# Optimization experiments

Hardware: AMD Instinct MI355X
Metric: run time of the kernel (lower is better)

The kernel has to match this reference:

```python
import jax, jax.numpy as jnp
import numpy as np

TOP_K = 2  # num_experts_per_tok


def setup_inputs() -> dict:
    key = jax.random.key(0)
    ks = jax.random.split(key, 4)
    B, S, H, I, E = 4, 2048, 2048, 4096, 8
    std = 0.02
    hidden_states = jax.random.normal(ks[0], (B, S, H), dtype=jnp.float32)
    gate_w = jax.random.normal(ks[1], (E, H), dtype=jnp.float32) * std   # nn.Linear weight [E,H]
    wfc = jax.random.normal(ks[2], (E, I, H), dtype=jnp.float32) * std   # c_fc weight [E,out,in]
    bfc = jnp.zeros((E, I), dtype=jnp.float32)                           # bias zero-init
    wproj = jax.random.normal(ks[3], (E, H, I), dtype=jnp.float32) * std # c_proj weight
    bproj = jnp.zeros((E, H), dtype=jnp.float32)
    return {"hidden_states": hidden_states, "gate_w": gate_w, "wfc": wfc,
            "bfc": bfc, "wproj": wproj, "bproj": bproj}


def reference(hidden_states, gate_w, wfc, bfc, wproj, bproj):
    B, S, H = hidden_states.shape
    E = wfc.shape[0]
    x = hidden_states.reshape(-1, H)                      # [T, H]
    router_logits = x @ gate_w.T                          # [T, E]
    top_vals, top_idx = jax.lax.top_k(router_logits, TOP_K)
    router_weights = jax.nn.softmax(top_vals.astype(jnp.float32), axis=-1).astype(x.dtype)  # [T, k]
    out = jnp.zeros_like(x)
    # Loop over the small fixed set of experts; each token contributes with its
    # combined gate weight for that expert (0 if not routed there). Same math as
    # the torch gather/grouped-GEMM/scatter-add path.
    for e in range(E):
        gate_e = jnp.sum(jnp.where(top_idx == e, router_weights, 0.0), axis=-1)  # [T]
        h = jax.nn.gelu(x @ wfc[e].T + bfc[e], approximate=False)                # [T, I]
        y = h @ wproj[e].T + bproj[e]                                            # [T, H]
        out = out + gate_e[:, None] * y
    return out.reshape(B, S, H), router_logits
```

## Files before the change

### kernel.cpp

```cpp
#include <hip/hip_runtime.h>
#include <hip/hip_bf16.h>
#include <math.h>

#define NT 8192
#define HD 2048
#define ID 4096
#define NE 8
#define MAXSLOT 17408
#define MAXRB 136

typedef __bf16 bf16x8 __attribute__((ext_vector_type(8)));
typedef float f32x4 __attribute__((ext_vector_type(4)));

__device__ __forceinline__ float bf2f(unsigned short u){
  union{unsigned u; float f;} v; v.u = ((unsigned)u) << 16; return v.f;
}

#define GLDS0(g, l) __builtin_amdgcn_global_load_lds( \
    (const __attribute__((address_space(1))) void*)(g), \
    (__attribute__((address_space(3))) void*)(l), 16, 0, 0)

__global__ __launch_bounds__(256) void cvt_kernel(const float* __restrict__ in,
                                                  __hip_bfloat16* __restrict__ outp, int n4){
  int i = blockIdx.x * blockDim.x + threadIdx.x;
  int stride = gridDim.x * blockDim.x;
  for (; i < n4; i += stride){
    float4 v = reinterpret_cast<const float4*>(in)[i];
    union{ushort4 u; __hip_bfloat16 h[4];} o;
    o.h[0] = __float2bfloat16(v.x); o.h[1] = __float2bfloat16(v.y);
    o.h[2] = __float2bfloat16(v.z); o.h[3] = __float2bfloat16(v.w);
    reinterpret_cast<ushort4*>(outp)[i] = o.u;
  }
}

__global__ __launch_bounds__(256) void router_kernel(
    const float* __restrict__ x, const float* __restrict__ gw,
    float* __restrict__ logits_out, int* __restrict__ tokExp,
    float* __restrict__ tokW, int* __restrict__ cnt)
{
  int wave = (blockIdx.x * blockDim.x + threadIdx.x) >> 6;
  int lane = threadIdx.x & 63;
  if (wave >= NT) return;
  const float* xr = x + (long)wave * HD;
  double acc[NE];
  #pragma unroll
  for (int e = 0; e < NE; e++) acc[e] = 0.0;
  for (int k = lane; k < HD; k += 64){
    double xv = (double)xr[k];
    #pragma unroll
    for (int e = 0; e < NE; e++) acc[e] += xv * (double)gw[e * HD + k];
  }
  #pragma unroll
  for (int e = 0; e < NE; e++){
    #pragma unroll
    for (int off = 32; off; off >>= 1) acc[e] += __shfl_down(acc[e], off, 64);
  }
  if (lane == 0){
    int e0 = 0; double v0 = acc[0];
    for (int e = 1; e < NE; e++) if (acc[e] > v0){ v0 = acc[e]; e0 = e; }
    int e1 = -1; double v1 = -1e300;
    for (int e = 0; e < NE; e++) if (e != e0 && acc[e] > v1){ v1 = acc[e]; e1 = e; }
    double ex = exp(v1 - v0);
    double s = 1.0 + ex;
    for (int e = 0; e < NE; e++) logits_out[wave * NE + e] = (float)acc[e];
    tokExp[wave * 2]     = e0; tokExp[wave * 2 + 1] = e1;
    tokW[wave * 2]       = (float)(1.0 / s);
    tokW[wave * 2 + 1]   = (float)(ex / s);
    atomicAdd(&cnt[e0], 1); atomicAdd(&cnt[e1], 1);
  }
}

__global__ void offsets_kernel(const int* __restrict__ cnt, int* __restrict__ padOff){
  if (threadIdx.x == 0 && blockIdx.x == 0){
    int o = 0;
    for (int e = 0; e < NE; e++){ padOff[e] = o; o += ((cnt[e] + 127) >> 7) << 7; }
    padOff[NE] = o;
  }
}

__global__ __launch_bounds__(256) void scatter_kernel(
    const int* __restrict__ tokExp, const float* __restrict__ tokW,
    const int* __restrict__ padOff, int* cursor,
    int* __restrict__ slotTok, int* __restrict__ tokSlot)
{
  int t = blockIdx.x * blockDim.x + threadIdx.x;
  if (t >= NT) return;
  #pragma unroll
  for (int s = 0; s < 2; s++){
    int e = tokExp[t * 2 + s];
    int pos = atomicAdd(&cursor[e], 1);
    int slot = padOff[e] + pos;
    slotTok[slot] = t;
    tokSlot[t * 2 + s] = slot;
  }
}

template<int GATHER_A, int EPI, int ND, int KD>
__global__ __launch_bounds__(256, 3) void moe_gemm_v12(
    const __hip_bfloat16* __restrict__ A,
    const __hip_bfloat16* __restrict__ W,
    const float* __restrict__ bias,
    const int* __restrict__ slotTok,
    const int* __restrict__ padOff,
    __hip_bfloat16* __restrict__ Yout)
{
  __shared__ __align__(16) __hip_bfloat16 lds[3 * 8192];
  const int rb = blockIdx.y;
  if (rb * 128 >= padOff[NE]) return;
  const int cb = blockIdx.x;
  int e = 0;
  #pragma unroll
  for (int i = 1; i < NE; i++) if (rb * 128 >= padOff[i]) e = i;

  const int tid  = threadIdx.x;
  const int lane = tid & 63;
  const int w    = tid >> 6;
  const int wr   = w >> 1, wc = w & 1;

  const int r16s = lane >> 2;
  const int cgs  = (lane & 3) ^ ((r16s >> 1) & 3);
  long aRow0, aRow1;
  {
    int g0 = rb * 128 + 32 * w + r16s, g1 = g0 + 16;
    if (GATHER_A){
      int t0 = slotTok[g0]; if (t0 < 0) t0 = 0;
      int t1 = slotTok[g1]; if (t1 < 0) t1 = 0;
      aRow0 = t0; aRow1 = t1;
    } else { aRow0 = g0; aRow1 = g1; }
  }
  const __hip_bfloat16* sA0 = A + aRow0 * (long)KD + cgs * 8;
  const __hip_bfloat16* sA1 = A + aRow1 * (long)KD + cgs * 8;
  const long bRow0 = (long)cb * 128 + 32 * w + r16s;
  const __hip_bfloat16* sB0 = W + (long)e * ND * KD + bRow0 * KD + cgs * 8;
  const __hip_bfloat16* sB1 = sB0 + 16 * (long)KD;

  __hip_bfloat16* dst0 = &lds[0 * 8192 + 2 * w * 512];
  __hip_bfloat16* dst1 = &lds[1 * 8192 + 2 * w * 512];
  __hip_bfloat16* dst2 = &lds[2 * 8192 + 2 * w * 512];

  const int r16f  = lane & 15;
  const int laneF = r16f * 32 + (((lane >> 4) ^ ((r16f >> 1) & 3))) * 8;
  const int adrA  = wr * 2048 + laneF;
  const int adrB  = 4096 + wc * 2048 + laneF;

  f32x4 acc[4][4] = {};

  constexpr int NKS = KD / 32;

#define STGADV(DP) do{ \
    GLDS0(sA0, (DP)); GLDS0(sA1, (DP) + 512); \
    GLDS0(sB0, (DP) + 4096); GLDS0(sB1, (DP) + 4096 + 512); \
    sA0 += 32; sA1 += 32; sB0 += 32; sB1 += 32; \
    asm volatile("" : "+v"(sA0), "+v"(sA1), "+v"(sB0), "+v"(sB1)); \
  }while(0)

#define RD_A(BUFC, M) (*reinterpret_cast<const bf16x8*>(&lds[(BUFC)*8192 + (M)*512 + adrA]))
#define RD_B(BUFC, N) (*reinterpret_cast<const bf16x8*>(&lds[(BUFC)*8192 + (N)*512 + adrB]))

#define BODY(K, BUFC, DP_STG) do{ \
    const int tt = t + (K); \
    if (tt < NKS){ \
      const bool dost = (tt + 2 < NKS); \
      if (dost){ STGADV(DP_STG); } \
      bf16x8 a0 = RD_A(BUFC,0), a1 = RD_A(BUFC,1), a2 = RD_A(BUFC,2), a3 = RD_A(BUFC,3); \
      bf16x8 b0 = RD_B(BUFC,0), b1 = RD_B(BUFC,1), b2 = RD_B(BUFC,2), b3 = RD_B(BUFC,3); \
      __builtin_amdgcn_s_setprio(1); \
      acc[0][0] = __builtin_amdgcn_mfma_f32_16x16x32_bf16(a0, b0, acc[0][0],0,0,0); \
      acc[1][0] = __builtin_amdgcn_mfma_f32_16x16x32_bf16(a1, b0, acc[1][0],0,0,0); \
      acc[2][0] = __builtin_amdgcn_mfma_f32_16x16x32_bf16(a2, b0, acc[2][0],0,0,0); \
      acc[3][0] = __builtin_amdgcn_mfma_f32_16x16x32_bf16(a3, b0, acc[3][0],0,0,0); \
      acc[0][1] = __builtin_amdgcn_mfma_f32_16x16x32_bf16(a0, b1, acc[0][1],0,0,0); \
      acc[1][1] = __builtin_amdgcn_mfma_f32_16x16x32_bf16(a1, b1, acc[1][1],0,0,0); \
      acc[2][1] = __builtin_amdgcn_mfma_f32_16x16x32_bf16(a2, b1, acc[2][1],0,0,0); \
      acc[3][1] = __builtin_amdgcn_mfma_f32_16x16x32_bf16(a3, b1, acc[3][1],0,0,0); \
      acc[0][2] = __builtin_amdgcn_mfma_f32_16x16x32_bf16(a0, b2, acc[0][2],0,0,0); \
      acc[1][2] = __builtin_amdgcn_mfma_f32_16x16x32_bf16(a1, b2, acc[1][2],0,0,0); \
      acc[2][2] = __builtin_amdgcn_mfma_f32_16x16x32_bf16(a2, b2, acc[2][2],0,0,0); \
      acc[3][2] = __builtin_amdgcn_mfma_f32_16x16x32_bf16(a3, b2, acc[3][2],0,0,0); \
      acc[0][3] = __builtin_amdgcn_mfma_f32_16x16x32_bf16(a0, b3, acc[0][3],0,0,0); \
      acc[1][3] = __builtin_amdgcn_mfma_f32_16x16x32_bf16(a1, b3, acc[1][3],0,0,0); \
      acc[2][3] = __builtin_amdgcn_mfma_f32_16x16x32_bf16(a2, b3, acc[2][3],0,0,0); \
      acc[3][3] = __builtin_amdgcn_mfma_f32_16x16x32_bf16(a3, b3, acc[3][3],0,0,0); \
      __builtin_amdgcn_s_setprio(0); \
      if (dost) asm volatile("s_waitcnt vmcnt(4)" ::: "memory"); \
      else      asm volatile("s_waitcnt vmcnt(0)" ::: "memory"); \
      __builtin_amdgcn_s_barrier(); \
    } \
  }while(0)

  STGADV(dst0);
  STGADV(dst1);
  asm volatile("s_waitcnt vmcnt(4)" ::: "memory");
  __builtin_amdgcn_s_barrier();

  for (int t = 0; t < NKS; t += 3){
    BODY(0, 0, dst2);
    BODY(1, 1, dst0);
    BODY(2, 2, dst1);
  }

  const int col0 = cb * 128 + wc * 64 + (lane & 15);
  const int row0 = rb * 128 + wr * 64 + (lane >> 4) * 4;
  #pragma unroll
  for (int n = 0; n < 4; n++){
    const int col = col0 + n * 16;
    const float bb = bias[(long)e * ND + col];
    #pragma unroll
    for (int m = 0; m < 4; m++){
      const long rbase = (long)(row0 + m * 16);
      #pragma unroll
      for (int r = 0; r < 4; r++){
        float v = acc[m][n][r] + bb;
        if (EPI == 0){
          float u = 0.7978845608f * (v + 0.044715f * v * v * v);
          float t2 = 1.0f - 2.0f / (__expf(2.0f * u) + 1.0f);
          v = 0.5f * v * (1.0f + t2);
        }
        Yout[(rbase + r) * ND + col] = __float2bfloat16(v);
      }
    }
  }
#undef STGADV
#undef RD_A
#undef RD_B
#undef BODY
}

__global__ __launch_bounds__(256) void combine_kernel(
    const __hip_bfloat16* __restrict__ yb,
    const int* __restrict__ tokSlot, const float* __restrict__ tokW,
    float* __restrict__ outp)
{
  const int t  = blockIdx.x;
  const int c0 = threadIdx.x * 8;
  const int s0 = tokSlot[t * 2], s1 = tokSlot[t * 2 + 1];
  const float w0 = tokW[t * 2], w1 = tokW[t * 2 + 1];
  const ushort4* p0 = reinterpret_cast<const ushort4*>(yb + (long)s0 * HD + c0);
  const ushort4* p1 = reinterpret_cast<const ushort4*>(yb + (long)s1 * HD + c0);
  float4 o[2];
  #pragma unroll
  for (int h = 0; h < 2; h++){
    ushort4 a = p0[h], b = p1[h];
    o[h].x = w0 * bf2f(a.x) + w1 * bf2f(b.x);
    o[h].y = w0 * bf2f(a.y) + w1 * bf2f(b.y);
    o[h].z = w0 * bf2f(a.z) + w1 * bf2f(b.z);
    o[h].w = w0 * bf2f(a.w) + w1 * bf2f(b.w);
  }
  float4* po = reinterpret_cast<float4*>(outp + (long)t * HD + c0);
  po[0] = o[0]; po[1] = o[1];
}

extern "C" void kernel_launch(void* const* d_in, const int* in_sizes, int n_in,
                              void* d_out, int out_size, void* d_ws, size_t ws_size,
                              hipStream_t stream)
{
  (void)in_sizes; (void)n_in; (void)out_size; (void)ws_size;
  const float* x     = (const float*)d_in[0];
  const float* gw    = (const float*)d_in[1];
  const float* wfc   = (const float*)d_in[2];
  const float* bfc   = (const float*)d_in[3];
  const float* wproj = (const float*)d_in[4];
  const float* bproj = (const float*)d_in[5];
  float* outp   = (float*)d_out;
  float* logits = outp + (size_t)NT * HD;

  char* ws = (char*)d_ws;
  size_t off = 0;
  auto alloc = [&](size_t b){ void* p = ws + off; off += (b + 255) & ~(size_t)255; return p; };

  char* shared0 = (char*)alloc((size_t)MAXSLOT * HD * 2);
  __hip_bfloat16* xb = (__hip_bfloat16*)shared0;
  __hip_bfloat16* yb = (__hip_bfloat16*)shared0;
  __hip_bfloat16* hb = (__hip_bfloat16*)alloc((size_t)MAXSLOT * ID * 2);
  int*   slotTok = (int*)alloc(MAXSLOT * 4);
  int*   tokExp  = (int*)alloc(NT * 2 * 4);
  float* tokW    = (float*)alloc(NT * 2 * 4);
  int*   tokSlot = (int*)alloc(NT * 2 * 4);
  int*   meta    = (int*)alloc(256);
  int* cnt = meta; int* cursor = meta + 8; int* padOff = meta + 16;

  __hip_bfloat16* wB = (__hip_bfloat16*)(ws + off);

  hipMemsetAsync(meta, 0, 256, stream);
  hipMemsetAsync(slotTok, 0xFF, MAXSLOT * 4, stream);

  cvt_kernel<<<2048, 256, 0, stream>>>(x, xb, NT * HD / 4);
  router_kernel<<<NT / 4, 256, 0, stream>>>(x, gw, logits, tokExp, tokW, cnt);
  offsets_kernel<<<1, 64, 0, stream>>>(cnt, padOff);
  scatter_kernel<<<NT / 256, 256, 0, stream>>>(tokExp, tokW, padOff, cursor, slotTok, tokSlot);

  cvt_kernel<<<2048, 256, 0, stream>>>(wfc, wB, NE * ID * HD / 4);
  moe_gemm_v12<1, 0, ID, HD><<<dim3(ID / 128, MAXRB), 256, 0, stream>>>(xb, wB, bfc, slotTok, padOff, hb);
  cvt_kernel<<<2048, 256, 0, stream>>>(wproj, wB, NE * HD * ID / 4);
  moe_gemm_v12<0, 1, HD, ID><<<dim3(HD / 128, MAXRB), 256, 0, stream>>>(hb, wB, bproj, slotTok, padOff, yb);

  combine_kernel<<<NT, 256, 0, stream>>>(yb, tokSlot, tokW, outp);
}
```

Measured before the change: 1.210 ms.

## Fuse fp32-to-bf16 weight conversion into MoE GEMM B-tile loading

Removes the separate weight conversion kernels and has the GEMM load fp32 weight tiles into registers, convert them to bf16 and write them into shared memory, with register double-buffering across a 6-step unrolled loop. This removes the full conversion passes over both expert weight tensors. In exchange each GEMM block reads twice as many weight bytes, uses more registers, and the main loop adds conversion ALU work and replaces explicit vmcnt waits with register dependencies.

Measured after the change: 1.231 ms. About the same (+1.8%).

```diff
diff --git a/kernel.cpp b/kernel.cpp
--- a/kernel.cpp
+++ b/kernel.cpp
@@ -96,9 +96,9 @@
 }
 
 template<int GATHER_A, int EPI, int ND, int KD>
-__global__ __launch_bounds__(256, 3) void moe_gemm_v12(
+__global__ __launch_bounds__(256, 3) void moe_gemm_fp(
     const __hip_bfloat16* __restrict__ A,
-    const __hip_bfloat16* __restrict__ W,
+    const float* __restrict__ Wf,
     const float* __restrict__ bias,
     const int* __restrict__ slotTok,
     const int* __restrict__ padOff,
@@ -130,13 +130,16 @@
   }
   const __hip_bfloat16* sA0 = A + aRow0 * (long)KD + cgs * 8;
   const __hip_bfloat16* sA1 = A + aRow1 * (long)KD + cgs * 8;
-  const long bRow0 = (long)cb * 128 + 32 * w + r16s;
-  const __hip_bfloat16* sB0 = W + (long)e * ND * KD + bRow0 * KD + cgs * 8;
-  const __hip_bfloat16* sB1 = sB0 + 16 * (long)KD;
 
   __hip_bfloat16* dst0 = &lds[0 * 8192 + 2 * w * 512];
   __hip_bfloat16* dst1 = &lds[1 * 8192 + 2 * w * 512];
   __hip_bfloat16* dst2 = &lds[2 * 8192 + 2 * w * 512];
+
+  const int r0   = lane >> 2;
+  const int cch  = lane & 3;
+  const float* bp0 = Wf + (long)e * ND * KD + ((long)cb * 128 + 32 * w + r0) * KD + cch * 8;
+  const float* bp1 = bp0 + 16 * (long)KD;
+  const int adrBW = 4096 + 2 * w * 512 + r0 * 32 + ((cch ^ ((r0 >> 1) & 3)) * 8);
 
   const int r16f  = lane & 15;
   const int laneF = r16f * 32 + (((lane >> 4) ^ ((r16f >> 1) & 3))) * 8;
@@ -147,23 +150,46 @@
 
   constexpr int NKS = KD / 32;
 
-#define STGADV(DP) do{ \
+#define STGA(DP) do{ \
     GLDS0(sA0, (DP)); GLDS0(sA1, (DP) + 512); \
-    GLDS0(sB0, (DP) + 4096); GLDS0(sB1, (DP) + 4096 + 512); \
-    sA0 += 32; sA1 += 32; sB0 += 32; sB1 += 32; \
-    asm volatile("" : "+v"(sA0), "+v"(sA1), "+v"(sB0), "+v"(sB1)); \
+    sA0 += 32; sA1 += 32; \
+    asm volatile("" : "+v"(sA0), "+v"(sA1)); \
+  }while(0)
+
+#define LOADB(L0,L1,L2,L3) do{ \
+    L0 = *reinterpret_cast<const float4*>(bp0); \
+    L1 = *reinterpret_cast<const float4*>(bp0 + 4); \
+    L2 = *reinterpret_cast<const float4*>(bp1); \
+    L3 = *reinterpret_cast<const float4*>(bp1 + 4); \
+    bp0 += 32; bp1 += 32; \
+    asm volatile("" ::: "memory"); \
+  }while(0)
+
+#define WRITEB(WBUF, W0,W1,W2,W3) do{ \
+    union{__hip_bfloat16 h[8]; float4 f;} pk0, pk1; \
+    pk0.h[0] = __float2bfloat16(W0.x); pk0.h[1] = __float2bfloat16(W0.y); \
+    pk0.h[2] = __float2bfloat16(W0.z); pk0.h[3] = __float2bfloat16(W0.w); \
+    pk0.h[4] = __float2bfloat16(W1.x); pk0.h[5] = __float2bfloat16(W1.y); \
+    pk0.h[6] = __float2bfloat16(W1.z); pk0.h[7] = __float2bfloat16(W1.w); \
+    pk1.h[0] = __float2bfloat16(W2.x); pk1.h[1] = __float2bfloat16(W2.y); \
+    pk1.h[2] = __float2bfloat16(W2.z); pk1.h[3] = __float2bfloat16(W2.w); \
+    pk1.h[4] = __float2bfloat16(W3.x); pk1.h[5] = __float2bfloat16(W3.y); \
+    pk1.h[6] = __float2bfloat16(W3.z); pk1.h[7] = __float2bfloat16(W3.w); \
+    *reinterpret_cast<float4*>(&lds[(WBUF) * 8192 + adrBW])       = pk0.f; \
+    *reinterpret_cast<float4*>(&lds[(WBUF) * 8192 + adrBW + 512]) = pk1.f; \
   }while(0)
 
 #define RD_A(BUFC, M) (*reinterpret_cast<const bf16x8*>(&lds[(BUFC)*8192 + (M)*512 + adrA]))
 #define RD_B(BUFC, N) (*reinterpret_cast<const bf16x8*>(&lds[(BUFC)*8192 + (N)*512 + adrB]))
 
-#define BODY(K, BUFC, DP_STG) do{ \
+#define BODY(K, BUFC, WBUF, DSTA, LA0,LA1,LA2,LA3, WA0,WA1,WA2,WA3) do{ \
     const int tt = t + (K); \
     if (tt < NKS){ \
-      const bool dost = (tt + 2 < NKS); \
-      if (dost){ STGADV(DP_STG); } \
+      if (tt + 2 < NKS){ STGA(DSTA); LOADB(LA0,LA1,LA2,LA3); } \
       bf16x8 a0 = RD_A(BUFC,0), a1 = RD_A(BUFC,1), a2 = RD_A(BUFC,2), a3 = RD_A(BUFC,3); \
       bf16x8 b0 = RD_B(BUFC,0), b1 = RD_B(BUFC,1), b2 = RD_B(BUFC,2), b3 = RD_B(BUFC,3); \
+      if (tt + 1 < NKS){ WRITEB(WBUF, WA0,WA1,WA2,WA3); } \
+      asm volatile("s_waitcnt lgkmcnt(0)" ::: "memory"); \
       __builtin_amdgcn_s_setprio(1); \
       acc[0][0] = __builtin_amdgcn_mfma_f32_16x16x32_bf16(a0, b0, acc[0][0],0,0,0); \
       acc[1][0] = __builtin_amdgcn_mfma_f32_16x16x32_bf16(a1, b0, acc[1][0],0,0,0); \
@@ -182,21 +208,27 @@
       acc[2][3] = __builtin_amdgcn_mfma_f32_16x16x32_bf16(a2, b3, acc[2][3],0,0,0); \
       acc[3][3] = __builtin_amdgcn_mfma_f32_16x16x32_bf16(a3, b3, acc[3][3],0,0,0); \
       __builtin_amdgcn_s_setprio(0); \
-      if (dost) asm volatile("s_waitcnt vmcnt(4)" ::: "memory"); \
-      else      asm volatile("s_waitcnt vmcnt(0)" ::: "memory"); \
       __builtin_amdgcn_s_barrier(); \
     } \
   }while(0)
 
-  STGADV(dst0);
-  STGADV(dst1);
-  asm volatile("s_waitcnt vmcnt(4)" ::: "memory");
+  float4 p0, p1, p2, p3, q0, q1, q2, q3;
+  LOADB(p0, p1, p2, p3);
+  STGA(dst0);
+  STGA(dst1);
+  LOADB(q0, q1, q2, q3);
+  WRITEB(0, p0, p1, p2, p3);
+  asm volatile("s_waitcnt vmcnt(6)" ::: "memory");
+  asm volatile("s_waitcnt lgkmcnt(0)" ::: "memory");
   __builtin_amdgcn_s_barrier();
 
-  for (int t = 0; t < NKS; t += 3){
-    BODY(0, 0, dst2);
-    BODY(1, 1, dst0);
-    BODY(2, 2, dst1);
+  for (int t = 0; t < NKS; t += 6){
+    BODY(0, 0, 1, dst2, p0,p1,p2,p3, q0,q1,q2,q3);
+    BODY(1, 1, 2, dst0, q0,q1,q2,q3, p0,p1,p2,p3);
+    BODY(2, 2, 0, dst1, p0,p1,p2,p3, q0,q1,q2,q3);
+    BODY(3, 0, 1, dst2, q0,q1,q2,q3, p0,p1,p2,p3);
+    BODY(4, 1, 2, dst0, p0,p1,p2,p3, q0,q1,q2,q3);
+    BODY(5, 2, 0, dst1, q0,q1,q2,q3, p0,p1,p2,p3);
   }
 
   const int col0 = cb * 128 + wc * 64 + (lane & 15);
@@ -220,7 +252,9 @@
       }
     }
   }
-#undef STGADV
+#undef STGA
+#undef LOADB
+#undef WRITEB
 #undef RD_A
 #undef RD_B
 #undef BODY
@@ -279,8 +313,6 @@
   int*   meta    = (int*)alloc(256);
   int* cnt = meta; int* cursor = meta + 8; int* padOff = meta + 16;
 
-  __hip_bfloat16* wB = (__hip_bfloat16*)(ws + off);
-
   hipMemsetAsync(meta, 0, 256, stream);
   hipMemsetAsync(slotTok, 0xFF, MAXSLOT * 4, stream);
 
@@ -289,10 +321,8 @@
   offsets_kernel<<<1, 64, 0, stream>>>(cnt, padOff);
   scatter_kernel<<<NT / 256, 256, 0, stream>>>(tokExp, tokW, padOff, cursor, slotTok, tokSlot);
 
-  cvt_kernel<<<2048, 256, 0, stream>>>(wfc, wB, NE * ID * HD / 4);
-  moe_gemm_v12<1, 0, ID, HD><<<dim3(ID / 128, MAXRB), 256, 0, stream>>>(xb, wB, bfc, slotTok, padOff, hb);
-  cvt_kernel<<<2048, 256, 0, stream>>>(wproj, wB, NE * HD * ID / 4);
-  moe_gemm_v12<0, 1, HD, ID><<<dim3(HD / 128, MAXRB), 256, 0, stream>>>(hb, wB, bproj, slotTok, padOff, yb);
+  moe_gemm_fp<1, 0, ID, HD><<<dim3(ID / 128, MAXRB), 256, 0, stream>>>(xb, wfc, bfc, slotTok, padOff, hb);
+  moe_gemm_fp<0, 1, HD, ID><<<dim3(HD / 128, MAXRB), 256, 0, stream>>>(hb, wproj, bproj, slotTok, padOff, yb);
 
   combine_kernel<<<NT, 256, 0, stream>>>(yb, tokSlot, tokW, outp);
 }
```
